# Kernel optimization log

Hardware: AMD Instinct MI355X
Metric: run time of the kernel (lower is better)

## Reference

```python
import jax, jax.numpy as jnp
import numpy as np

# snntorch default ATan surrogate (alpha=2): fwd = heaviside, bwd = g / (1 + (pi*x)^2)
@jax.custom_vjp
def atan_spike(x):
    return (x > 0).astype(x.dtype)

def _atan_fwd(x):
    return atan_spike(x), x

def _atan_bwd(x, g):
    return (g / (1.0 + (jnp.pi * x) ** 2),)

atan_spike.defvjp(_atan_fwd, _atan_bwd)

B = 4096  # batch
D = 100   # row length / fc1 in-features; also number of timesteps (rows)
O = 3     # fc1 out-features

def setup_inputs() -> dict:
    key = jax.random.key(0)
    k1, k2, k3, k4 = jax.random.split(key, 4)
    x = jax.random.uniform(k1, (B, D, D), jnp.float32)   # rate-coding probabilities
    u = jax.random.uniform(k2, (B, D, D), jnp.float32)   # Bernoulli uniforms for rate coding
    lim = 1.0 / np.sqrt(D)
    W = jax.random.uniform(k3, (O, D), jnp.float32, -lim, lim)
    b = jax.random.uniform(k4, (O,), jnp.float32, -lim, lim)
    beta = jnp.float32(0.95)
    threshold = jnp.float32(1.0)
    return {"x": x, "u": u, "W": W, "b": b, "beta": beta, "threshold": threshold}

def reference(x, u, W, b, beta, threshold):
    # sgen.rate(x, 1)[0]: one-step Bernoulli rate coding, prob = x
    spikes = (u < x).astype(x.dtype)            # [B, 100, 100]
    seq = jnp.transpose(spikes, (1, 0, 2))      # [T=100, B, 100] (loop over rows)

    def step(mem, inp):                          # mem: [B, 3], inp: [B, 100]
        cur = inp @ W.T + b                      # fc1
        # snntorch Leaky, reset_mechanism='subtract': reset from previous mem, detached
        reset = jax.lax.stop_gradient(atan_spike(mem - threshold))
        mem = beta * mem + cur - reset * threshold
        spk = atan_spike(mem - threshold)
        return mem, (spk, mem)

    mem0 = jnp.zeros((x.shape[0], O), x.dtype)   # init_leaky()
    _, (spk_rec, mem_rec) = jax.lax.scan(step, mem0, seq)
    return spk_rec, mem_rec                      # each [100, B, 3]
```

## Files before the change

kernel.cpp:

```cpp
#include <hip/hip_runtime.h>

#define NB 4096
#define ND 100
#define NT 100
#define NO 3
#define PITCH 101

__global__ __launch_bounds__(384) void cur_kernel(
    const float* __restrict__ x, const float* __restrict__ u,
    const float* __restrict__ W, const float* __restrict__ bias,
    float* __restrict__ cur_out)
{
    __shared__ float sp[NT * PITCH];
    __shared__ float Ws[NO * PITCH];
    __shared__ float bs[NO];

    const int b   = blockIdx.x;
    const int tid = threadIdx.x;

    if (tid < NO * ND) {
        int o = tid / ND;
        int d = tid - o * ND;
        Ws[o * PITCH + d] = W[tid];
    }
    if (tid < NO) bs[tid] = bias[tid];

    const float4* x4 = (const float4*)(x + (size_t)b * (ND * ND));
    const float4* u4 = (const float4*)(u + (size_t)b * (ND * ND));
    for (int i = tid; i < (ND * ND) / 4; i += 384) {
        float4 xv = x4[i];
        float4 uv = u4[i];
        int f   = i * 4;
        int row = f / ND;
        int col = f - row * ND;
        float* p = &sp[row * PITCH + col];
        p[0] = (uv.x < xv.x) ? 1.0f : 0.0f;
        p[1] = (uv.y < xv.y) ? 1.0f : 0.0f;
        p[2] = (uv.z < xv.z) ? 1.0f : 0.0f;
        p[3] = (uv.w < xv.w) ? 1.0f : 0.0f;
    }
    __syncthreads();

    if (tid < NO * NT) {
        int o = tid / NT;
        int t = tid - o * NT;
        const float* sr = &sp[t * PITCH];
        const float* wr = &Ws[o * PITCH];
        float acc = bs[o];
#pragma unroll 10
        for (int d = 0; d < ND; ++d)
            acc = fmaf(sr[d], wr[d], acc);
        cur_out[(size_t)b * (NT * NO) + t * NO + o] = acc;
    }
}

__global__ __launch_bounds__(64) void scan_kernel(
    const float* __restrict__ cur,
    const float* __restrict__ beta_p, const float* __restrict__ thr_p,
    float* __restrict__ out)
{
    const int tid = blockIdx.x * 64 + threadIdx.x;
    const int b = tid / NO;
    const int o = tid - b * NO;
    const float beta = beta_p[0];
    const float thr  = thr_p[0];

    const float* c = cur + (size_t)b * (NT * NO) + o;
    float* mem_rec = out + (size_t)NT * NB * NO;

    float mem = 0.0f;
#pragma unroll 5
    for (int t = 0; t < NT; ++t) {
        float cv = c[t * NO];
        float rsub = (mem > thr) ? thr : 0.0f;
        mem = __fadd_rn(__fadd_rn(__fmul_rn(beta, mem), cv), -rsub);
        float s = (mem > thr) ? 1.0f : 0.0f;
        out[(size_t)t * (NB * NO) + tid]      = s;
        mem_rec[(size_t)t * (NB * NO) + tid]  = mem;
    }
}

extern "C" void kernel_launch(void* const* d_in, const int* in_sizes, int n_in,
                              void* d_out, int out_size, void* d_ws, size_t ws_size,
                              hipStream_t stream) {
    const float* x    = (const float*)d_in[0];
    const float* u    = (const float*)d_in[1];
    const float* W    = (const float*)d_in[2];
    const float* bias = (const float*)d_in[3];
    const float* beta = (const float*)d_in[4];
    const float* thr  = (const float*)d_in[5];
    float* out = (float*)d_out;

    float* cur_ws = (float*)d_ws;

    cur_kernel<<<NB, 384, 0, stream>>>(x, u, W, bias, cur_ws);
    scan_kernel<<<(NB * NO) / 64, 64, 0, stream>>>(cur_ws, beta, thr, out);
}
```

Baseline: 349.4 us.

## Fuse spike encoding, fc1 and leaky scan into one kernel

Merges the current-computation and scan kernels into a single kernel per batch element. Each block computes fc1 with 32-lane groups that load one row of x/u as float4, hold W in registers, and reduce with xor shuffles, then writes the currents to a small shared buffer. Three threads then run the 100-step scan and write spikes and membrane values directly. This removes the global workspace round trip and the second launch, but the serial scan now runs on only 3 threads per block, and its stores are strided across blocks.

```diff
diff --git a/kernel.cpp b/kernel.cpp
--- a/kernel.cpp
+++ b/kernel.cpp
@@ -4,79 +4,76 @@
 #define ND 100
 #define NT 100
 #define NO 3
-#define PITCH 101
 
-__global__ __launch_bounds__(384) void cur_kernel(
+__global__ __launch_bounds__(320) void fused_leaky(
     const float* __restrict__ x, const float* __restrict__ u,
     const float* __restrict__ W, const float* __restrict__ bias,
-    float* __restrict__ cur_out)
+    const float* __restrict__ beta_p, const float* __restrict__ thr_p,
+    float* __restrict__ out)
 {
-    __shared__ float sp[NT * PITCH];
-    __shared__ float Ws[NO * PITCH];
-    __shared__ float bs[NO];
+    __shared__ float cur_s[NT * 4];
 
     const int b   = blockIdx.x;
     const int tid = threadIdx.x;
+    const int hw  = tid >> 5;
+    const int l   = tid & 31;
 
-    if (tid < NO * ND) {
-        int o = tid / ND;
-        int d = tid - o * ND;
-        Ws[o * PITCH + d] = W[tid];
+    float4 w0 = {0,0,0,0}, w1 = {0,0,0,0}, w2 = {0,0,0,0};
+    if (l < 25) {
+        w0 = ((const float4*)(W         ))[l];
+        w1 = ((const float4*)(W +    ND))[l];
+        w2 = ((const float4*)(W + 2*ND ))[l];
     }
-    if (tid < NO) bs[tid] = bias[tid];
 
-    const float4* x4 = (const float4*)(x + (size_t)b * (ND * ND));
-    const float4* u4 = (const float4*)(u + (size_t)b * (ND * ND));
-    for (int i = tid; i < (ND * ND) / 4; i += 384) {
-        float4 xv = x4[i];
-        float4 uv = u4[i];
-        int f   = i * 4;
-        int row = f / ND;
-        int col = f - row * ND;
-        float* p = &sp[row * PITCH + col];
-        p[0] = (uv.x < xv.x) ? 1.0f : 0.0f;
-        p[1] = (uv.y < xv.y) ? 1.0f : 0.0f;
-        p[2] = (uv.z < xv.z) ? 1.0f : 0.0f;
-        p[3] = (uv.w < xv.w) ? 1.0f : 0.0f;
+    const float* xb = x + (size_t)b * (ND * ND);
+    const float* ub = u + (size_t)b * (ND * ND);
+
+    for (int iter = 0; iter < 10; ++iter) {
+        const int t = hw + 10 * iter;
+        float a0 = 0.f, a1 = 0.f, a2 = 0.f;
+        if (l < 25) {
+            const float4 xv = ((const float4*)(xb + t * ND))[l];
+            const float4 uv = ((const float4*)(ub + t * ND))[l];
+            const float s0 = (uv.x < xv.x) ? 1.f : 0.f;
+            const float s1 = (uv.y < xv.y) ? 1.f : 0.f;
+            const float s2 = (uv.z < xv.z) ? 1.f : 0.f;
+            const float s3 = (uv.w < xv.w) ? 1.f : 0.f;
+            a0 = fmaf(s3, w0.w, fmaf(s2, w0.z, fmaf(s1, w0.y, s0 * w0.x)));
+            a1 = fmaf(s3, w1.w, fmaf(s2, w1.z, fmaf(s1, w1.y, s0 * w1.x)));
+            a2 = fmaf(s3, w2.w, fmaf(s2, w2.z, fmaf(s1, w2.y, s0 * w2.x)));
+        }
+        #pragma unroll
+        for (int m = 1; m < 32; m <<= 1) {
+            a0 += __shfl_xor(a0, m);
+            a1 += __shfl_xor(a1, m);
+            a2 += __shfl_xor(a2, m);
+        }
+        if (l == 0) {
+            cur_s[t * 4 + 0] = a0;
+            cur_s[t * 4 + 1] = a1;
+            cur_s[t * 4 + 2] = a2;
+        }
     }
     __syncthreads();
 
-    if (tid < NO * NT) {
-        int o = tid / NT;
-        int t = tid - o * NT;
-        const float* sr = &sp[t * PITCH];
-        const float* wr = &Ws[o * PITCH];
-        float acc = bs[o];
-#pragma unroll 10
-        for (int d = 0; d < ND; ++d)
-            acc = fmaf(sr[d], wr[d], acc);
-        cur_out[(size_t)b * (NT * NO) + t * NO + o] = acc;
-    }
-}
+    if (tid < NO) {
+        const int   o    = tid;
+        const float beta = beta_p[0];
+        const float thr  = thr_p[0];
+        const float bo   = bias[o];
+        const int   col  = b * NO + o;
+        float* mem_rec = out + (size_t)NT * NB * NO;
 
-__global__ __launch_bounds__(64) void scan_kernel(
-    const float* __restrict__ cur,
-    const float* __restrict__ beta_p, const float* __restrict__ thr_p,
-    float* __restrict__ out)
-{
-    const int tid = blockIdx.x * 64 + threadIdx.x;
-    const int b = tid / NO;
-    const int o = tid - b * NO;
-    const float beta = beta_p[0];
-    const float thr  = thr_p[0];
-
-    const float* c = cur + (size_t)b * (NT * NO) + o;
-    float* mem_rec = out + (size_t)NT * NB * NO;
-
-    float mem = 0.0f;
-#pragma unroll 5
-    for (int t = 0; t < NT; ++t) {
-        float cv = c[t * NO];
-        float rsub = (mem > thr) ? thr : 0.0f;
-        mem = __fadd_rn(__fadd_rn(__fmul_rn(beta, mem), cv), -rsub);
-        float s = (mem > thr) ? 1.0f : 0.0f;
-        out[(size_t)t * (NB * NO) + tid]      = s;
-        mem_rec[(size_t)t * (NB * NO) + tid]  = mem;
+        float mem = 0.f;
+        #pragma unroll 4
+        for (int t = 0; t < NT; ++t) {
+            const float cv   = cur_s[t * 4 + o] + bo;
+            const float rsub = (mem > thr) ? thr : 0.f;
+            mem = __fadd_rn(__fadd_rn(__fmul_rn(beta, mem), cv), -rsub);
+            const float s = (mem > thr) ? 1.f : 0.f;
+            out[(size_t)t * (NB * NO) + col]     = s;
+            mem_rec[(size_t)t * (NB * NO) + col] = mem;
+        }
     }
 }
 
@@ -91,8 +88,5 @@
     const float* thr  = (const float*)d_in[5];
     float* out = (float*)d_out;
 
-    float* cur_ws = (float*)d_ws;
-
-    cur_kernel<<<NB, 384, 0, stream>>>(x, u, W, bias, cur_ws);
-    scan_kernel<<<(NB * NO) / 64, 64, 0, stream>>>(cur_ws, beta, thr, out);
+    fused_leaky<<<NB, 320, 0, stream>>>(x, u, W, bias, beta, thr, out);
 }
```

Result: no change. 355.2 us (+1.7%).
